# Kernel optimization log

Measured on AMD Instinct MI355X. Metric: run time of the kernel, lower is better.

The kernel has to match this reference:

```python
import math
import jax, jax.numpy as jnp
import numpy as np

T = 4096
D_MODEL = 1024
NUM_HEADS = 16
HEAD_DIM = D_MODEL // NUM_HEADS


def setup_inputs() -> dict:
    key = jax.random.key(0)
    k_x, k_wqkv, k_wproj = jax.random.split(key, 3)
    # match eqx.nn.Linear init scale: U(-1/sqrt(in), 1/sqrt(in)); randn*small works too,
    # but keep magnitudes reasonable so softmax isn't saturated.
    s_in = 1.0 / math.sqrt(D_MODEL)
    x = jax.random.normal(k_x, (T, D_MODEL), dtype=jnp.float32)
    W_qkv = jax.random.normal(k_wqkv, (3 * D_MODEL, D_MODEL), dtype=jnp.float32) * s_in
    b_qkv = jnp.zeros((3 * D_MODEL,), dtype=jnp.float32)
    W_proj = jax.random.normal(k_wproj, (D_MODEL, D_MODEL), dtype=jnp.float32) * s_in
    b_proj = jnp.zeros((D_MODEL,), dtype=jnp.float32)
    return {"x": x, "W_qkv": W_qkv, "b_qkv": b_qkv, "W_proj": W_proj, "b_proj": b_proj}


def reference(x, W_qkv, b_qkv, W_proj, b_proj):
    T_, C = x.shape  # (seq, d_model)
    H, hd = NUM_HEADS, HEAD_DIM
    # c_attn: eqx Linear computes W @ x + b per token -> x @ W.T + b
    qkv = x @ W_qkv.T + b_qkv  # (T, 3C)
    q, k, v = jnp.split(qkv, 3, axis=1)
    # (T, C) -> (H, T, hd)
    q = q.reshape(T_, H, hd).swapaxes(0, 1)
    k = k.reshape(T_, H, hd).swapaxes(0, 1)
    v = v.reshape(T_, H, hd).swapaxes(0, 1)
    scores = jnp.einsum("htd,hsd->hts", q, k) / math.sqrt(hd)  # (H, T, T)
    causal = jnp.tril(jnp.ones((T_, T_), dtype=bool))
    scores = jnp.where(causal, scores, -jnp.inf)
    attn = jax.nn.softmax(scores, axis=-1)
    y = jnp.einsum("hts,hsd->htd", attn, v)  # (H, T, hd)
    y = y.swapaxes(0, 1).reshape(T_, C)
    y = y @ W_proj.T + b_proj
    return y
```

## Files before the change

### kernel.cpp

```cpp
#include <hip/hip_runtime.h>
#include <math.h>
#include <string.h>

#define T_SEQ 4096
#define DM 1024
#define NH 16
#define HD 64

typedef short s8v __attribute__((ext_vector_type(8)));
typedef float f4v __attribute__((ext_vector_type(4)));

__device__ inline unsigned short f2bf(float f) {
    unsigned u; memcpy(&u, &f, 4);
    u = u + 0x7fffu + ((u >> 16) & 1u);
    return (unsigned short)(u >> 16);
}

__device__ inline float bf2f(unsigned short s) {
    unsigned u = (unsigned)s << 16;
    float f; memcpy(&f, &u, 4);
    return f;
}

__device__ inline float exp2fn(float x) {
#if __has_builtin(__builtin_amdgcn_exp2f)
    return __builtin_amdgcn_exp2f(x);
#else
    return exp2f(x);
#endif
}

__device__ inline void gld_lds16(const void* g, void* l) {
    __builtin_amdgcn_global_load_lds(
        (const __attribute__((address_space(1))) void*)g,
        (__attribute__((address_space(3))) void*)l, 16, 0, 0);
}

__global__ __launch_bounds__(256)
void cvt3(const float* __restrict__ i0, unsigned short* __restrict__ o0, int n0,
          const float* __restrict__ i1, unsigned short* __restrict__ o1, int n1,
          const float* __restrict__ i2, unsigned short* __restrict__ o2, int n2) {
    int i = blockIdx.x * 256 + threadIdx.x;
    const float* in; unsigned short* out; int j;
    if (i < n0)           { in = i0; out = o0; j = i; }
    else if (i < n0 + n1) { in = i1; out = o1; j = i - n0; }
    else if (i < n0 + n1 + n2) { in = i2; out = o2; j = i - n0 - n1; }
    else return;
    const float4* p = (const float4*)(in + (size_t)j * 8);
    float4 a = p[0], b = p[1];
    unsigned short o[8] = {f2bf(a.x), f2bf(a.y), f2bf(a.z), f2bf(a.w),
                           f2bf(b.x), f2bf(b.y), f2bf(b.z), f2bf(b.w)};
    uint4 pk; memcpy(&pk, o, 16);
    *(uint4*)(out + (size_t)j * 8) = pk;
}

template<int MODE, int TN>
__global__ __launch_bounds__(256)
void gemm_bt_mfma(const unsigned short* __restrict__ A, const unsigned short* __restrict__ B,
                  const float* __restrict__ bias, void* __restrict__ Cout,
                  unsigned short* __restrict__ qbuf, unsigned short* __restrict__ kbuf2,
                  unsigned short* __restrict__ vT,
                  int M, int N, int K) {
    constexpr int NF = TN / 32;
    __shared__ __align__(16) short As[4096];
    __shared__ __align__(16) short Bs[TN * 32];
    const int tid = threadIdx.x;
    const int w = tid >> 6, lane = tid & 63;
    const int wr = w >> 1, wc = w & 1;
    const int m0 = blockIdx.y * 128, n0 = blockIdx.x * TN;

    const bool doA = (w < 2);
    const bool doStage = doA || ((w & 1) * 64 < TN);
    const unsigned short* src = doA ? A : B;
    const int rbase = (doA ? m0 : n0) + (w & 1) * 64;
    const unsigned short* gsrc = src + (size_t)(rbase + (lane & 15)) * K + ((lane >> 4) * 8);
    short* ldst = (doA ? As : Bs) + ((w & 1) * 4) * 512;

    f4v acc[4][NF];
    #pragma unroll
    for (int i = 0; i < 4; ++i)
        #pragma unroll
        for (int j = 0; j < NF; ++j) acc[i][j] = (f4v){0.f, 0.f, 0.f, 0.f};

    for (int k0 = 0; k0 < K; k0 += 32) {
        __syncthreads();
        if (doStage) {
            #pragma unroll
            for (int i = 0; i < 4; ++i)
                gld_lds16(gsrc + (size_t)(i * 16) * K + k0, ldst + i * 512);
        }
        __syncthreads();

        s8v af[4], bf[NF];
        #pragma unroll
        for (int i = 0; i < 4; ++i) af[i] = *(const s8v*)&As[((wr * 4 + i) * 64 + lane) * 8];
        #pragma unroll
        for (int j = 0; j < NF; ++j) bf[j] = *(const s8v*)&Bs[((wc * NF + j) * 64 + lane) * 8];
        #pragma unroll
        for (int i = 0; i < 4; ++i)
            #pragma unroll
            for (int j = 0; j < NF; ++j)
                acc[i][j] = __builtin_amdgcn_mfma_f32_16x16x32_bf16(af[i], bf[j], acc[i][j], 0, 0, 0);
    }

    const int l15 = lane & 15, quad = lane >> 4;
    float bj[NF];
    #pragma unroll
    for (int j = 0; j < NF; ++j) bj[j] = bias[n0 + wc * (TN / 2) + j * 16 + l15];

    if (MODE == 2 && n0 >= 2 * DM) {
        #pragma unroll
        for (int i = 0; i < 4; ++i) {
            int tb = m0 + wr * 64 + i * 16 + quad * 4;
            #pragma unroll
            for (int j = 0; j < NF; ++j) {
                int dg = n0 - 2 * DM + wc * (TN / 2) + j * 16 + l15;
                unsigned short o[4];
                #pragma unroll
                for (int rg = 0; rg < 4; ++rg) o[rg] = f2bf(acc[i][j][rg] + bj[j]);
                unsigned long long pk; memcpy(&pk, o, 8);
                *(unsigned long long*)&vT[(size_t)dg * T_SEQ + tb] = pk;
            }
        }
    } else if (MODE == 2) {
        unsigned short* dst = (n0 < DM) ? qbuf : kbuf2;
        const int nb = (n0 < DM) ? n0 : n0 - DM;
        #pragma unroll
        for (int i = 0; i < 4; ++i) {
            #pragma unroll
            for (int rg = 0; rg < 4; ++rg) {
                int row = m0 + wr * 64 + i * 16 + quad * 4 + rg;
                #pragma unroll
                for (int j = 0; j < NF; ++j) {
                    int col = nb + wc * (TN / 2) + j * 16 + l15;
                    dst[(size_t)row * DM + col] = f2bf(acc[i][j][rg] + bj[j]);
                }
            }
        }
    } else {
        #pragma unroll
        for (int i = 0; i < 4; ++i) {
            #pragma unroll
            for (int rg = 0; rg < 4; ++rg) {
                int row = m0 + wr * 64 + i * 16 + quad * 4 + rg;
                #pragma unroll
                for (int j = 0; j < NF; ++j) {
                    int col = n0 + wc * (TN / 2) + j * 16 + l15;
                    ((float*)Cout)[(size_t)row * N + col] = acc[i][j][rg] + bj[j];
                }
            }
        }
    }
}

__device__ __forceinline__ void soft_step(f4v* st, bool diag, int qloc, int quad, int l15,
                                          float& lr, short* pw) {
    const float C2  = 0.1803368851f;
    const float MC2 = 12.0f * 0.1803368851f;
    float sv[4][4];
    #pragma unroll
    for (int kb = 0; kb < 4; ++kb)
        #pragma unroll
        for (int rg = 0; rg < 4; ++rg) {
            float s = st[kb][rg];
            if (diag && (kb * 16 + quad * 4 + rg > qloc)) s = -3.0e38f;
            float t = exp2fn(fmaf(s, C2, -MC2));
            sv[kb][rg] = t;
            lr += t;
        }
    #pragma unroll
    for (int kb = 0; kb < 4; ++kb) {
        unsigned u0 = __float_as_uint(sv[kb][0]) + 0x8000u;
        unsigned u1 = __float_as_uint(sv[kb][1]) + 0x8000u;
        unsigned u2 = __float_as_uint(sv[kb][2]) + 0x8000u;
        unsigned u3 = __float_as_uint(sv[kb][3]) + 0x8000u;
        int2 v;
        v.x = (int)__builtin_amdgcn_perm(u1, u0, 0x07060302);
        v.y = (int)__builtin_amdgcn_perm(u3, u2, 0x07060302);
        int c = (kb >> 1) * 64 + ((kb & 1) * 2 + (quad >> 1)) * 16 + l15;
        c ^= ((c >> 3) & 7);
        *(int2*)&pw[c * 8 + (quad & 1) * 4] = v;
    }
}

__global__ __launch_bounds__(256, 3)
void attn_mfma6(const unsigned short* __restrict__ qb,
                const unsigned short* __restrict__ kbf,
                const unsigned short* __restrict__ vT,
                unsigned short* __restrict__ y0,
                unsigned short* __restrict__ y1,
                unsigned short* __restrict__ y2,
                float* __restrict__ lsum) {
    const int b = blockIdx.x;
    const int par = b % 3;
    const int idx = b / 3;
    const int h = idx & 15, a = idx >> 4;
    const int tid = threadIdx.x;
    const int w = tid >> 6, lane = tid & 63;
    const int quad = lane >> 4, l15 = lane & 15;
    const int cq = h * HD, hv = h * HD;
    unsigned short* ypar = (par == 0) ? y0 : (par == 1) ? y1 : y2;
    float* lpar = lsum + ((size_t)par * NH + h) * T_SEQ;

    __shared__ short KB[2][4096];
    __shared__ short VTs[2][4096];
    __shared__ short QP[8192];

    for (int ph = 0; ph < 2; ++ph) {
        const int qt = ph ? (31 - a) : a;
        const int q0 = qt * 128;
        const int kmax = 2 * qt + 1;
        const int nk = (kmax >= par) ? (kmax - par) / 3 + 1 : 0;
        const int kt0 = par * 64;

        __syncthreads();
        #pragma unroll
        for (int rr = 0; rr < 4; ++rr) {
            int ch = rr * 256 + tid;
            int qg = ch >> 7, hf = (ch >> 6) & 1, ln = ch & 63;
            gld_lds16(qb + (size_t)(q0 + qg * 16 + (ln & 15)) * DM + cq + hf * 32 + ((ln >> 4) << 3),
                      &QP[(ch & ~63) * 8]);
        }
        if (nk > 0) {
            #pragma unroll
            for (int rr = 0; rr < 2; ++rr) {
                int ch = rr * 256 + tid;
                int blk = ch >> 7, hf = (ch >> 6) & 1, ln = ch & 63;
                gld_lds16(kbf + (size_t)(kt0 + blk * 16 + (ln & 15)) * DM + cq + hf * 32 + ((ln >> 4) << 3),
                          &KB[0][(ch & ~63) * 8]);
                gld_lds16(vT + (size_t)(hv + blk * 16 + (ln & 15)) * T_SEQ + kt0 + hf * 32 + ((ln >> 4) << 3),
                          &VTs[0][(ch & ~63) * 8]);
            }
        }
        __syncthreads();

        s8v qf[2][2];
        #pragma unroll
        for (int g = 0; g < 2; ++g)
            #pragma unroll
            for (int hf = 0; hf < 2; ++hf)
                qf[g][hf] = *(const s8v*)&QP[((((g * 4 + w) * 2 + hf) * 64) + lane) * 8];
        __syncthreads();

        f4v O0[4], O1[4];
        #pragma unroll
        for (int ob = 0; ob < 4; ++ob) {
            O0[ob] = (f4v){0.f, 0.f, 0.f, 0.f};
            O1[ob] = (f4v){0.f, 0.f, 0.f, 0.f};
        }
        float lr0 = 0.f, lr1 = 0.f;

        for (int i = 0; i < nk; ++i) {
            const int kt = par + 3 * i;
            const int p = i & 1;
            const bool g0a = (kt <= 2 * qt);
            const bool m0 = (kt == 2 * qt);
            const bool m1 = (kt == 2 * qt + 1);
            if (i < nk - 1) {
                const int k1 = kt0 + (i + 1) * 192;
                #pragma unroll
                for (int rr = 0; rr < 2; ++rr) {
                    int ch = rr * 256 + tid;
                    int blk = ch >> 7, hf = (ch >> 6) & 1, ln = ch & 63;
                    gld_lds16(kbf + (size_t)(k1 + blk * 16 + (ln & 15)) * DM + cq
                                  + hf * 32 + ((ln >> 4) << 3),
                              &KB[p ^ 1][(ch & ~63) * 8]);
                    gld_lds16(vT + (size_t)(hv + blk * 16 + (ln & 15)) * T_SEQ + k1
                                  + hf * 32 + ((ln >> 4) << 3),
                              &VTs[p ^ 1][(ch & ~63) * 8]);
                }
            }

            f4v st0[4], st1[4];
            #pragma unroll
            for (int kb = 0; kb < 4; ++kb) {
                s8v k0f = *(const s8v*)&KB[p][((kb * 2 + 0) * 64 + lane) * 8];
                s8v k1f = *(const s8v*)&KB[p][((kb * 2 + 1) * 64 + lane) * 8];
                f4v c1 = (f4v){0.f, 0.f, 0.f, 0.f};
                c1 = __builtin_amdgcn_mfma_f32_16x16x32_bf16(k0f, qf[1][0], c1, 0, 0, 0);
                c1 = __builtin_amdgcn_mfma_f32_16x16x32_bf16(k1f, qf[1][1], c1, 0, 0, 0);
                st1[kb] = c1;
                if (g0a) {
                    f4v c0 = (f4v){0.f, 0.f, 0.f, 0.f};
                    c0 = __builtin_amdgcn_mfma_f32_16x16x32_bf16(k0f, qf[0][0], c0, 0, 0, 0);
                    c0 = __builtin_amdgcn_mfma_f32_16x16x32_bf16(k1f, qf[0][1], c0, 0, 0, 0);
                    st0[kb] = c0;
                }
            }

            short* PB = QP;
            if (g0a) soft_step(st0, m0, w * 16 + l15, quad, l15, lr0, &PB[(w * 2 + 0) * 1024]);
            soft_step(st1, m1, w * 16 + l15, quad, l15, lr1, &PB[(w * 2 + 1) * 1024]);

            asm volatile("s_waitcnt lgkmcnt(0)" ::: "memory");
            int c0i = lane ^ ((lane >> 3) & 7);
            s8v pf10 = *(const s8v*)&PB[(w * 2 + 1) * 1024 + c0i * 8];
            s8v pf11 = *(const s8v*)&PB[(w * 2 + 1) * 1024 + (64 + c0i) * 8];
            s8v pf00, pf01;
            if (g0a) {
                pf00 = *(const s8v*)&PB[(w * 2 + 0) * 1024 + c0i * 8];
                pf01 = *(const s8v*)&PB[(w * 2 + 0) * 1024 + (64 + c0i) * 8];
            }

            #pragma unroll
            for (int ob = 0; ob < 4; ++ob) {
                s8v v0f = *(const s8v*)&VTs[p][((ob * 2 + 0) * 64 + lane) * 8];
                s8v v1f = *(const s8v*)&VTs[p][((ob * 2 + 1) * 64 + lane) * 8];
                O1[ob] = __builtin_amdgcn_mfma_f32_16x16x32_bf16(v0f, pf10, O1[ob], 0, 0, 0);
                O1[ob] = __builtin_amdgcn_mfma_f32_16x16x32_bf16(v1f, pf11, O1[ob], 0, 0, 0);
                if (g0a) {
                    O0[ob] = __builtin_amdgcn_mfma_f32_16x16x32_bf16(v0f, pf00, O0[ob], 0, 0, 0);
                    O0[ob] = __builtin_amdgcn_mfma_f32_16x16x32_bf16(v1f, pf01, O0[ob], 0, 0, 0);
                }
            }
            __syncthreads();
        }

        lr0 += __shfl_xor(lr0, 16); lr0 += __shfl_xor(lr0, 32);
        lr1 += __shfl_xor(lr1, 16); lr1 += __shfl_xor(lr1, 32);
        #pragma unroll
        for (int g = 0; g < 2; ++g) {
            const f4v* O = g ? O1 : O0;
            int qrow = q0 + g * 64 + w * 16 + l15;
            size_t ybase = (size_t)qrow * DM + cq;
            #pragma unroll
            for (int ob = 0; ob < 4; ++ob) {
                unsigned short o[4];
                #pragma unroll
                for (int rg = 0; rg < 4; ++rg) o[rg] = f2bf(O[ob][rg]);
                unsigned long long pk; memcpy(&pk, o, 8);
                *(unsigned long long*)&ypar[ybase + ob * 16 + quad * 4] = pk;
            }
            if (quad == 0) lpar[qrow] = g ? lr1 : lr0;
        }
    }
}

__global__ __launch_bounds__(256)
void attn_combine3(const unsigned short* __restrict__ y0,
                   const unsigned short* __restrict__ y1,
                   const unsigned short* __restrict__ y2,
                   const float* __restrict__ lsum,
                   unsigned short* __restrict__ yout) {
    int i = blockIdx.x * 256 + threadIdx.x;
    int t = i >> 7, d8 = i & 127;
    int h = d8 >> 3;
    float l = lsum[(size_t)h * T_SEQ + t]
            + lsum[((size_t)NH + h) * T_SEQ + t]
            + lsum[((size_t)2 * NH + h) * T_SEQ + t];
    float inv = 1.f / l;
    size_t off = (size_t)t * DM + d8 * 8;
    uint4 ua = *(const uint4*)(y0 + off);
    uint4 ub = *(const uint4*)(y1 + off);
    uint4 uc = *(const uint4*)(y2 + off);
    const unsigned short* pa = (const unsigned short*)&ua;
    const unsigned short* pb = (const unsigned short*)&ub;
    const unsigned short* pc = (const unsigned short*)&uc;
    unsigned short o[8];
    #pragma unroll
    for (int k = 0; k < 8; ++k)
        o[k] = f2bf((bf2f(pa[k]) + bf2f(pb[k]) + bf2f(pc[k])) * inv);
    uint4 pk; memcpy(&pk, o, 16);
    *(uint4*)(yout + off) = pk;
}

extern "C" void kernel_launch(void* const* d_in, const int* in_sizes, int n_in,
                              void* d_out, int out_size, void* d_ws, size_t ws_size,
                              hipStream_t stream) {
    const float* x     = (const float*)d_in[0];
    const float* Wqkv  = (const float*)d_in[1];
    const float* bqkv  = (const float*)d_in[2];
    const float* Wproj = (const float*)d_in[3];
    const float* bproj = (const float*)d_in[4];
    float* out = (float*)d_out;

    char* ws = (char*)d_ws;
    unsigned short* qbuf  = (unsigned short*)(ws);
    unsigned short* kbuf  = (unsigned short*)(ws + ( 8u << 20));
    unsigned short* vTb   = (unsigned short*)(ws + (16u << 20));
    unsigned short* yattb = (unsigned short*)(ws + (24u << 20));
    unsigned short* wprjb = (unsigned short*)(ws + (32u << 20));
    float*          lsum  = (float*)         (ws + (34u << 20));
    unsigned short* xb    = (unsigned short*)(ws + (35u << 20));
    unsigned short* wqkvb = (unsigned short*)(ws + (43u << 20));
    unsigned short* y0p   = (unsigned short*)(ws + (35u << 20));
    unsigned short* y1p   = (unsigned short*)(ws + (43u << 20));
    unsigned short* y2p   = (unsigned short*)(ws + (51u << 20));

    dim3 blk(256);
    {
        int n0 = T_SEQ * DM / 8, n1 = 3 * DM * DM / 8, n2 = DM * DM / 8;
        cvt3<<<dim3((n0 + n1 + n2 + 255) / 256), blk, 0, stream>>>(
            x, xb, n0, Wqkv, wqkvb, n1, Wproj, wprjb, n2);
    }
    gemm_bt_mfma<2, 128><<<dim3(3 * DM / 128, T_SEQ / 128), blk, 0, stream>>>(
        xb, wqkvb, bqkv, nullptr, qbuf, kbuf, vTb, T_SEQ, 3 * DM, DM);
    attn_mfma6<<<dim3(768), blk, 0, stream>>>(qbuf, kbuf, vTb, y0p, y1p, y2p, lsum);
    attn_combine3<<<dim3(T_SEQ * DM / 8 / 256), blk, 0, stream>>>(y0p, y1p, y2p, lsum, yattb);
    gemm_bt_mfma<0, 64><<<dim3(DM / 64, T_SEQ / 128), blk, 0, stream>>>(
        yattb, wprjb, bproj, out, nullptr, nullptr, nullptr, T_SEQ, DM, DM);
}
```

Before: 231.9 us.

## Keep softmax probabilities in registers and pre-tile V into MFMA fragment layout

The QKV GEMM epilogue now writes V in a per-head, per-64-token tile layout that matches the attention kernel's MFMA fragment order, so each V tile load becomes a contiguous copy. The softmax probabilities are packed straight into registers as MFMA operands instead of taking a round trip through LDS with a swizzled write and read plus an lgkmcnt wait. The barrier after the Q fragment load is dropped because QP is no longer reused as the P scratch buffer. This relies on the key permutation being consistent between the P register layout and the pre-tiled V fragments.

```diff
diff --git a/kernel.cpp b/kernel.cpp
--- a/kernel.cpp
+++ b/kernel.cpp
@@ -109,17 +109,19 @@
     for (int j = 0; j < NF; ++j) bj[j] = bias[n0 + wc * (TN / 2) + j * 16 + l15];
 
     if (MODE == 2 && n0 >= 2 * DM) {
+        const int tile = (m0 + wr * 64) >> 6;
+        const int hh = ((n0 - 2 * DM) >> 6) + wc;
         #pragma unroll
         for (int i = 0; i < 4; ++i) {
-            int tb = m0 + wr * 64 + i * 16 + quad * 4;
             #pragma unroll
             for (int j = 0; j < NF; ++j) {
-                int dg = n0 - 2 * DM + wc * (TN / 2) + j * 16 + l15;
                 unsigned short o[4];
                 #pragma unroll
                 for (int rg = 0; rg < 4; ++rg) o[rg] = f2bf(acc[i][j][rg] + bj[j]);
                 unsigned long long pk; memcpy(&pk, o, 8);
-                *(unsigned long long*)&vT[(size_t)dg * T_SEQ + tb] = pk;
+                size_t off = (size_t)hh * 262144 + (size_t)tile * 4096
+                           + (size_t)((j * 2 + (i >> 1)) * 64 + lane) * 8 + (i & 1) * 4;
+                *(unsigned long long*)&vT[off] = pk;
             }
         }
     } else if (MODE == 2) {
@@ -153,8 +155,8 @@
     }
 }
 
-__device__ __forceinline__ void soft_step(f4v* st, bool diag, int qloc, int quad, int l15,
-                                          float& lr, short* pw) {
+__device__ __forceinline__ void soft_step(f4v* st, bool diag, int qloc, int quad,
+                                          float& lr, s8v& pf0, s8v& pf1) {
     const float C2  = 0.1803368851f;
     const float MC2 = 12.0f * 0.1803368851f;
     float sv[4][4];
@@ -168,23 +170,24 @@
             sv[kb][rg] = t;
             lr += t;
         }
+    int pk[4][2];
     #pragma unroll
     for (int kb = 0; kb < 4; ++kb) {
         unsigned u0 = __float_as_uint(sv[kb][0]) + 0x8000u;
         unsigned u1 = __float_as_uint(sv[kb][1]) + 0x8000u;
         unsigned u2 = __float_as_uint(sv[kb][2]) + 0x8000u;
         unsigned u3 = __float_as_uint(sv[kb][3]) + 0x8000u;
-        int2 v;
-        v.x = (int)__builtin_amdgcn_perm(u1, u0, 0x07060302);
-        v.y = (int)__builtin_amdgcn_perm(u3, u2, 0x07060302);
-        int c = (kb >> 1) * 64 + ((kb & 1) * 2 + (quad >> 1)) * 16 + l15;
-        c ^= ((c >> 3) & 7);
-        *(int2*)&pw[c * 8 + (quad & 1) * 4] = v;
-    }
+        pk[kb][0] = (int)__builtin_amdgcn_perm(u1, u0, 0x07060302);
+        pk[kb][1] = (int)__builtin_amdgcn_perm(u3, u2, 0x07060302);
+    }
+    int4 a = {pk[0][0], pk[0][1], pk[1][0], pk[1][1]};
+    int4 b = {pk[2][0], pk[2][1], pk[3][0], pk[3][1]};
+    memcpy(&pf0, &a, 16);
+    memcpy(&pf1, &b, 16);
 }
 
 __global__ __launch_bounds__(256, 3)
-void attn_mfma6(const unsigned short* __restrict__ qb,
+void attn_mfma7(const unsigned short* __restrict__ qb,
                 const unsigned short* __restrict__ kbf,
                 const unsigned short* __restrict__ vT,
                 unsigned short* __restrict__ y0,
@@ -198,13 +201,14 @@
     const int tid = threadIdx.x;
     const int w = tid >> 6, lane = tid & 63;
     const int quad = lane >> 4, l15 = lane & 15;
-    const int cq = h * HD, hv = h * HD;
+    const int cq = h * HD;
     unsigned short* ypar = (par == 0) ? y0 : (par == 1) ? y1 : y2;
     float* lpar = lsum + ((size_t)par * NH + h) * T_SEQ;
+    const unsigned short* vbase = vT + (size_t)h * 262144;
 
     __shared__ short KB[2][4096];
     __shared__ short VTs[2][4096];
-    __shared__ short QP[8192];
+    __shared__ short QB[8192];
 
     for (int ph = 0; ph < 2; ++ph) {
         const int qt = ph ? (31 - a) : a;
@@ -219,7 +223,7 @@
             int ch = rr * 256 + tid;
             int qg = ch >> 7, hf = (ch >> 6) & 1, ln = ch & 63;
             gld_lds16(qb + (size_t)(q0 + qg * 16 + (ln & 15)) * DM + cq + hf * 32 + ((ln >> 4) << 3),
-                      &QP[(ch & ~63) * 8]);
+                      &QB[(ch & ~63) * 8]);
         }
         if (nk > 0) {
             #pragma unroll
@@ -228,7 +232,7 @@
                 int blk = ch >> 7, hf = (ch >> 6) & 1, ln = ch & 63;
                 gld_lds16(kbf + (size_t)(kt0 + blk * 16 + (ln & 15)) * DM + cq + hf * 32 + ((ln >> 4) << 3),
                           &KB[0][(ch & ~63) * 8]);
-                gld_lds16(vT + (size_t)(hv + blk * 16 + (ln & 15)) * T_SEQ + kt0 + hf * 32 + ((ln >> 4) << 3),
+                gld_lds16(vbase + (size_t)(kt0 >> 6) * 4096 + (size_t)ch * 8,
                           &VTs[0][(ch & ~63) * 8]);
             }
         }
@@ -239,8 +243,7 @@
         for (int g = 0; g < 2; ++g)
             #pragma unroll
             for (int hf = 0; hf < 2; ++hf)
-                qf[g][hf] = *(const s8v*)&QP[((((g * 4 + w) * 2 + hf) * 64) + lane) * 8];
-        __syncthreads();
+                qf[g][hf] = *(const s8v*)&QB[((((g * 4 + w) * 2 + hf) * 64) + lane) * 8];
 
         f4v O0[4], O1[4];
         #pragma unroll
@@ -265,8 +268,7 @@
                     gld_lds16(kbf + (size_t)(k1 + blk * 16 + (ln & 15)) * DM + cq
                                   + hf * 32 + ((ln >> 4) << 3),
                               &KB[p ^ 1][(ch & ~63) * 8]);
-                    gld_lds16(vT + (size_t)(hv + blk * 16 + (ln & 15)) * T_SEQ + k1
-                                  + hf * 32 + ((ln >> 4) << 3),
+                    gld_lds16(vbase + (size_t)(k1 >> 6) * 4096 + (size_t)ch * 8,
                               &VTs[p ^ 1][(ch & ~63) * 8]);
                 }
             }
@@ -288,19 +290,9 @@
                 }
             }
 
-            short* PB = QP;
-            if (g0a) soft_step(st0, m0, w * 16 + l15, quad, l15, lr0, &PB[(w * 2 + 0) * 1024]);
-            soft_step(st1, m1, w * 16 + l15, quad, l15, lr1, &PB[(w * 2 + 1) * 1024]);
-
-            asm volatile("s_waitcnt lgkmcnt(0)" ::: "memory");
-            int c0i = lane ^ ((lane >> 3) & 7);
-            s8v pf10 = *(const s8v*)&PB[(w * 2 + 1) * 1024 + c0i * 8];
-            s8v pf11 = *(const s8v*)&PB[(w * 2 + 1) * 1024 + (64 + c0i) * 8];
-            s8v pf00, pf01;
-            if (g0a) {
-                pf00 = *(const s8v*)&PB[(w * 2 + 0) * 1024 + c0i * 8];
-                pf01 = *(const s8v*)&PB[(w * 2 + 0) * 1024 + (64 + c0i) * 8];
-            }
+            s8v pf10, pf11, pf00, pf01;
+            soft_step(st1, m1, w * 16 + l15, quad, lr1, pf10, pf11);
+            if (g0a) soft_step(st0, m0, w * 16 + l15, quad, lr0, pf00, pf01);
 
             #pragma unroll
             for (int ob = 0; ob < 4; ++ob) {
@@ -395,7 +387,7 @@
     }
     gemm_bt_mfma<2, 128><<<dim3(3 * DM / 128, T_SEQ / 128), blk, 0, stream>>>(
         xb, wqkvb, bqkv, nullptr, qbuf, kbuf, vTb, T_SEQ, 3 * DM, DM);
-    attn_mfma6<<<dim3(768), blk, 0, stream>>>(qbuf, kbuf, vTb, y0p, y1p, y2p, lsum);
+    attn_mfma7<<<dim3(768), blk, 0, stream>>>(qbuf, kbuf, vTb, y0p, y1p, y2p, lsum);
     attn_combine3<<<dim3(T_SEQ * DM / 8 / 256), blk, 0, stream>>>(y0p, y1p, y2p, lsum, yattb);
     gemm_bt_mfma<0, 64><<<dim3(DM / 64, T_SEQ / 128), blk, 0, stream>>>(
         yattb, wprjb, bproj, out, nullptr, nullptr, nullptr, T_SEQ, DM, DM);
```

Result: faster. 218.5 us (-5.8%).
